# Performance work log

Hardware: AMD Instinct MI355X
Metric: run time of the kernel (lower is better)

## Reference

```python
import jax, jax.numpy as jnp
import numpy as np

# Sheet geometry: 256x256 neurons, 32 random synapses + 1 self synapse per neuron
R, C, S, STD, B = 256, 256, 32, 10.0, 64
N = R * C
NNZ = N * (S + 1)


def _build_indices(seed=0):
    """Replicates the torch constructor: per neuron (i,j), draw S gaussian
    2D offsets (std=STD), truncate to int, clamp to the sheet, linearize as
    i*C + j, and append the neuron's own index (self synapse).
    A[row=synapse, col=root] so out = A @ x^T scatters into synapse locations.
    """
    rng = np.random.default_rng(seed)
    ii, jj = np.meshgrid(np.arange(R), np.arange(C), indexing='ij')
    centers = np.stack([ii.ravel(), jj.ravel()], axis=1)           # [N, 2]
    syn = (rng.standard_normal((N, 2, S)) * STD
           + centers[:, :, None]).astype(np.int64)                 # trunc like .long()
    syn[:, 0] = np.clip(syn[:, 0], 0, R - 1)
    syn[:, 1] = np.clip(syn[:, 1], 0, C - 1)
    lin = syn[:, 0] * C + syn[:, 1]                                # [N, S]
    rows = np.concatenate([lin, np.arange(N)[:, None]], axis=1).ravel()  # [NNZ]
    cols = np.repeat(np.arange(N), S + 1)                          # [NNZ]
    return rows, cols


def setup_inputs() -> dict:
    key = jax.random.key(0)
    k1, k2 = jax.random.split(key)
    rows, cols = _build_indices()
    # He initialization: randn * sqrt(2 / synapses_per_neuron)
    values = jax.random.normal(k1, (NNZ,), dtype=jnp.float32) * np.float32(np.sqrt(2.0 / S))
    x = jax.random.normal(k2, (B, N), dtype=jnp.float32)  # batch_first
    return {"x": x, "values": values,
            "rows": jnp.asarray(rows, dtype=jnp.int64 if jax.config.jax_enable_x64 else jnp.int32),
            "cols": jnp.asarray(cols, dtype=jnp.int64 if jax.config.jax_enable_x64 else jnp.int32)}


def reference(x, values, rows, cols):
    # Sparse mm: out = A @ x^T with A[rows[e], cols[e]] += values[e]
    # (coalescing duplicates in torch_sparse sums values; segment_sum is equivalent)
    xt = x.T                                   # [N, B]
    gathered = xt[cols]                        # [NNZ, B] gather by root neuron
    out = jax.ops.segment_sum(values[:, None] * gathered, rows,
                              num_segments=N)  # [N, B] scatter to synapse rows
    return out.T                               # back to batch_first [B, N]
```

## Files before the change

### kernel.cpp

```cpp
#include <hip/hip_runtime.h>
#include <stdint.h>

#define N_NEUR  65536
#define NNZ_E   2162688
#define NBUK    4096
#define BSH     4
#define BROWS   16
#define EPB     4096
#define NBLK_E  (NNZ_E / EPB)
#define CHUNK   1536
#define EBUFSZ  (CHUNK + BROWS * 8)


__device__ inline unsigned short f2bf(float f) {
  const uint32_t u = __float_as_uint(f);
  return (unsigned short)((u + 0x7FFFu + ((u >> 16) & 1u)) >> 16);
}

__global__ __launch_bounds__(256) void k_front(const float* __restrict__ x,
                                               unsigned short* __restrict__ xtb,
                                               const int* __restrict__ rows,
                                               int* __restrict__ bcnt) {
  __shared__ float smem[64 * 65];
  const int t = threadIdx.x;
  if (blockIdx.x < 1024) {
    float (*tile)[65] = (float (*)[65])smem;
    const int n0 = blockIdx.x * 64;
    const int lane = t & 63;
    const int w = t >> 6;
    #pragma unroll
    for (int bb = w; bb < 64; bb += 4)
      tile[bb][lane] = x[(size_t)bb * N_NEUR + n0 + lane];
    __syncthreads();
    #pragma unroll
    for (int nn = w; nn < 64; nn += 4)
      xtb[(size_t)(n0 + nn) * 64 + lane] = f2bf(tile[lane][nn]);
  } else {
    int* lh = (int*)smem;
    #pragma unroll
    for (int q = 0; q < NBUK / 256; ++q) lh[q * 256 + t] = 0;
    __syncthreads();
    const int e0 = (blockIdx.x - 1024) * EPB;
    #pragma unroll
    for (int k = 0; k < EPB / 256; ++k)
      atomicAdd(&lh[rows[e0 + k * 256 + t] >> BSH], 1);
    __syncthreads();
    #pragma unroll
    for (int q = 0; q < NBUK / 256; ++q) {
      const int v = lh[q * 256 + t];
      if (v) atomicAdd(&bcnt[q * 256 + t], v);
    }
  }
}

__device__ inline int wave_incl_scan(int v, int lane) {
  #pragma unroll
  for (int off = 1; off < 64; off <<= 1) {
    int tv = __shfl_up(v, off, 64);
    if (lane >= off) v += tv;
  }
  return v;
}

__global__ __launch_bounds__(256) void k_bscan(const int* __restrict__ bcnt,
                                               int* __restrict__ boffs,
                                               int* __restrict__ gcur) {
  const int t = threadIdx.x, lane = t & 63, w = t >> 6;
  int c[16], s = 0;
  #pragma unroll
  for (int k = 0; k < 16; ++k) { c[k] = bcnt[t * 16 + k]; s += c[k]; }
  int incl = wave_incl_scan(s, lane);
  __shared__ int wsum[4];
  if (lane == 63) wsum[w] = incl;
  __syncthreads();
  int base = 0;
  for (int i = 0; i < w; ++i) base += wsum[i];
  int run = base + incl - s;
  #pragma unroll
  for (int k = 0; k < 16; ++k) {
    boffs[t * 16 + k] = run;
    gcur[t * 16 + k]  = run;
    run += c[k];
  }
}

__global__ __launch_bounds__(256) void k_bin(const int* __restrict__ rows,
                                             const float* __restrict__ vals,
                                             int* __restrict__ gcur,
                                             uint64_t* __restrict__ csr) {
  __shared__ int lc[NBUK];
  __shared__ int lofs[NBUK];
  __shared__ int wsum[4];
  __shared__ uint64_t ebuf[EPB];
  const int t = threadIdx.x, lane = t & 63, w = t >> 6;
  #pragma unroll
  for (int q = 0; q < NBUK / 256; ++q) lc[q * 256 + t] = 0;
  __syncthreads();
  const int e0 = blockIdx.x * EPB;
  int rcache[EPB / 256];
  #pragma unroll
  for (int k = 0; k < EPB / 256; ++k) {
    const int r = rows[e0 + k * 256 + t];
    rcache[k] = r;
    atomicAdd(&lc[r >> BSH], 1);
  }
  __syncthreads();
  {
    int c[16], s = 0;
    #pragma unroll
    for (int k = 0; k < 16; ++k) { c[k] = lc[t * 16 + k]; s += c[k]; }
    int incl = wave_incl_scan(s, lane);
    if (lane == 63) wsum[w] = incl;
    __syncthreads();
    int base = 0;
    for (int i = 0; i < w; ++i) base += wsum[i];
    int run = base + incl - s;
    #pragma unroll
    for (int k = 0; k < 16; ++k) { lofs[t * 16 + k] = run; run += c[k]; }
  }
  __syncthreads();
  #pragma unroll
  for (int q = 0; q < NBUK / 256; ++q) {
    const int bb = q * 256 + t;
    const int c = lc[bb];
    if (c) lc[bb] = atomicAdd(&gcur[bb], c) - lofs[bb];
  }
  __syncthreads();
  #pragma unroll
  for (int k = 0; k < EPB / 256; ++k) {
    const int e = e0 + k * 256 + t;
    const int r = rcache[k];
    const uint32_t c = (uint32_t)e / 33u;
    const uint64_t pk = ((uint64_t)__float_as_uint(vals[e]) << 32) |
                        ((uint32_t)r << 16) | c;
    const int pos = atomicAdd(&lofs[r >> BSH], 1);
    ebuf[pos] = pk;
  }
  __syncthreads();
  #pragma unroll
  for (int k = 0; k < EPB / 256; ++k) {
    const int idx = k * 256 + t;
    const uint64_t pk = ebuf[idx];
    const int bb = (int)((pk >> (16 + BSH)) & (NBUK - 1));
    csr[lc[bb] + idx] = pk;
  }
}

__global__ __launch_bounds__(256) void k_gather(const unsigned short* __restrict__ xtb,
                                                const int* __restrict__ boffs,
                                                const int* __restrict__ bcnt,
                                                const uint64_t* __restrict__ csr,
                                                float* __restrict__ out) {
  __shared__ uint64_t ebuf[EBUFSZ];
  __shared__ float tile[BROWS][66];
  __shared__ int lhist[BROWS], lofs[BROWS], lcur[BROWS], lpc[BROWS];
  const int t = threadIdx.x, lane = t & 63, w = t >> 6;
  const int h = lane >> 5, p = lane & 31;
  const int bid = blockIdx.x;
  const int g = (bid & 7) * (NBUK / 8) + (bid >> 3);
  const int r0 = g * BROWS;
  const int beg = boffs[g];
  const int cnt = bcnt[g];
  const uint32_t* __restrict__ xtu = (const uint32_t*)xtb;

  float accx[4] = {0.f, 0.f, 0.f, 0.f};
  float accy[4] = {0.f, 0.f, 0.f, 0.f};

  for (int c0 = 0; c0 < cnt; c0 += CHUNK) {
    const int len = (cnt - c0 < CHUNK) ? (cnt - c0) : CHUNK;
    if (t < BROWS) lhist[t] = 0;
    __syncthreads();
    uint64_t E[CHUNK / 256];
    #pragma unroll
    for (int u = 0; u < CHUNK / 256; ++u) {
      const int i = u * 256 + t;
      if (i < len) {
        const uint64_t e = csr[beg + c0 + i];
        E[u] = e;
        atomicAdd(&lhist[(int)((e >> 16) & (BROWS - 1))], 1);
      }
    }
    __syncthreads();
    if (t == 0) {
      int run = 0;
      #pragma unroll
      for (int r = 0; r < BROWS; ++r) {
        const int c = lhist[r];
        const int pc = (c + 7) & ~7;
        lofs[r] = run; lcur[r] = run; lpc[r] = pc;
        run += pc;
      }
    }
    __syncthreads();
    if (t < 128) {
      const int r = t >> 3, pi = t & 7;
      const int c = lhist[r];
      if (pi < lpc[r] - c) ebuf[lofs[r] + c + pi] = 0ULL;
    }
    #pragma unroll
    for (int u = 0; u < CHUNK / 256; ++u) {
      const int i = u * 256 + t;
      if (i < len) {
        const int rlo = (int)((E[u] >> 16) & (BROWS - 1));
        const int pos = atomicAdd(&lcur[rlo], 1);
        ebuf[pos] = E[u];
      }
    }
    __syncthreads();
    #pragma unroll
    for (int q = 0; q < 4; ++q) {
      const int rlo = w * 4 + q;
      const int s = __builtin_amdgcn_readfirstlane(lofs[rlo]);
      const int npair = __builtin_amdgcn_readfirstlane(lpc[rlo]) >> 1;
      float ax = 0.f, ay = 0.f, bx = 0.f, by = 0.f;
      int ti = 0;
      for (; ti + 8 <= npair; ti += 8) {
        uint64_t e[8]; uint32_t xv[8];
        #pragma unroll
        for (int u = 0; u < 8; ++u) e[u] = ebuf[s + 2 * (ti + u) + h];
        #pragma unroll
        for (int u = 0; u < 8; ++u)
          xv[u] = xtu[(int)(e[u] & 0xFFFF) * 32 + p];
        #pragma unroll
        for (int u = 0; u < 8; ++u) {
          const float v  = __uint_as_float((uint32_t)(e[u] >> 32));
          const float lo = __uint_as_float(xv[u] << 16);
          const float hi = __uint_as_float(xv[u] & 0xFFFF0000u);
          if (u & 1) { bx = fmaf(v, lo, bx); by = fmaf(v, hi, by); }
          else       { ax = fmaf(v, lo, ax); ay = fmaf(v, hi, ay); }
        }
      }
      if (ti < npair) {
        uint64_t e[4]; uint32_t xv[4];
        #pragma unroll
        for (int u = 0; u < 4; ++u) e[u] = ebuf[s + 2 * (ti + u) + h];
        #pragma unroll
        for (int u = 0; u < 4; ++u)
          xv[u] = xtu[(int)(e[u] & 0xFFFF) * 32 + p];
        #pragma unroll
        for (int u = 0; u < 4; ++u) {
          const float v  = __uint_as_float((uint32_t)(e[u] >> 32));
          const float lo = __uint_as_float(xv[u] << 16);
          const float hi = __uint_as_float(xv[u] & 0xFFFF0000u);
          if (u & 1) { bx = fmaf(v, lo, bx); by = fmaf(v, hi, by); }
          else       { ax = fmaf(v, lo, ax); ay = fmaf(v, hi, ay); }
        }
      }
      accx[q] += ax + bx;
      accy[q] += ay + by;
    }
    __syncthreads();
  }

  #pragma unroll
  for (int q = 0; q < 4; ++q) {
    float sx = accx[q] + __shfl_xor(accx[q], 32, 64);
    float sy = accy[q] + __shfl_xor(accy[q], 32, 64);
    if (h == 0) {
      tile[w * 4 + q][2 * p]     = sx;
      tile[w * 4 + q][2 * p + 1] = sy;
    }
  }
  __syncthreads();
  #pragma unroll
  for (int pp = 0; pp < (BROWS * 64) / 256; ++pp) {
    const int idx = pp * 256 + t;
    const int bb = idx >> 4;
    const int rl = idx & (BROWS - 1);
    out[(size_t)bb * N_NEUR + r0 + rl] = tile[rl][bb];
  }
}

extern "C" void kernel_launch(void* const* d_in, const int* in_sizes, int n_in,
                              void* d_out, int out_size, void* d_ws, size_t ws_size,
                              hipStream_t stream) {
  const float* x    = (const float*)d_in[0];
  const float* vals = (const float*)d_in[1];
  const int*   rows = (const int*)d_in[2];
  float* out = (float*)d_out;

  char* ws = (char*)d_ws;
  unsigned short* xtb = (unsigned short*)(ws + 0);
  int*      bcnt  = (int*)     (ws + 16777216);
  int*      boffs = (int*)     (ws + 16793600);
  int*      gcur  = (int*)     (ws + 16809984);
  uint64_t* csr   = (uint64_t*)(ws + 16826368);

  hipMemsetAsync(bcnt, 0, NBUK * sizeof(int), stream);
  k_front<<<1024 + NBLK_E, 256, 0, stream>>>(x, xtb, rows, bcnt);
  k_bscan<<<1, 256, 0, stream>>>(bcnt, boffs, gcur);
  k_bin<<<NBLK_E, 256, 0, stream>>>(rows, vals, gcur, csr);
  k_gather<<<NBUK, 256, 0, stream>>>(xtb, boffs, bcnt, csr, out);
}
```

Measured before the change: 88.30 us.

## Split row sort into separate kernel, fold bucket scan into binning, balance gather waves

The global bucket scan is folded into every k_bin block, which removes the single-block k_bscan launch. A new k_bin2 kernel sorts each bucket's edges by row into a padded csr2 array. k_gather then streams presorted entries with 128-bit loads and splits the work evenly across its four waves, flushing per-row partial sums through shared-memory atomics. Buckets are also mapped to blocks in an interleaved front/back order. The aims are to cut the sort and sync overhead inside the gather and to balance load across waves, at the cost of an extra kernel pass over the edges. There is also a new risk: k_bin2 clamps buckets to CAP (4096) entries, so larger buckets would silently drop edges.

```diff
diff --git a/kernel.cpp b/kernel.cpp
--- a/kernel.cpp
+++ b/kernel.cpp
@@ -8,13 +8,18 @@
 #define BROWS   16
 #define EPB     4096
 #define NBLK_E  (NNZ_E / EPB)
-#define CHUNK   1536
-#define EBUFSZ  (CHUNK + BROWS * 8)
+#define CAP     4096
 
 
 __device__ inline unsigned short f2bf(float f) {
   const uint32_t u = __float_as_uint(f);
   return (unsigned short)((u + 0x7FFFu + ((u >> 16) & 1u)) >> 16);
+}
+
+__device__ inline int bucket_of_block(int bid) {
+  const int l = bid >> 3;
+  const int lf = (l & 1) ? (511 - (l >> 1)) : (l >> 1);
+  return (bid & 7) * 512 + lf;
 }
 
 __global__ __launch_bounds__(256) void k_front(const float* __restrict__ x,
@@ -62,37 +67,42 @@
   return v;
 }
 
-__global__ __launch_bounds__(256) void k_bscan(const int* __restrict__ bcnt,
-                                               int* __restrict__ boffs,
-                                               int* __restrict__ gcur) {
-  const int t = threadIdx.x, lane = t & 63, w = t >> 6;
-  int c[16], s = 0;
-  #pragma unroll
-  for (int k = 0; k < 16; ++k) { c[k] = bcnt[t * 16 + k]; s += c[k]; }
-  int incl = wave_incl_scan(s, lane);
-  __shared__ int wsum[4];
-  if (lane == 63) wsum[w] = incl;
-  __syncthreads();
-  int base = 0;
-  for (int i = 0; i < w; ++i) base += wsum[i];
-  int run = base + incl - s;
-  #pragma unroll
-  for (int k = 0; k < 16; ++k) {
-    boffs[t * 16 + k] = run;
-    gcur[t * 16 + k]  = run;
-    run += c[k];
-  }
-}
-
 __global__ __launch_bounds__(256) void k_bin(const int* __restrict__ rows,
                                              const float* __restrict__ vals,
+                                             const int* __restrict__ bcnt,
+                                             int* __restrict__ boffs,
                                              int* __restrict__ gcur,
-                                             uint64_t* __restrict__ csr) {
+                                             uint64_t* __restrict__ csr1) {
   __shared__ int lc[NBUK];
   __shared__ int lofs[NBUK];
   __shared__ int wsum[4];
   __shared__ uint64_t ebuf[EPB];
   const int t = threadIdx.x, lane = t & 63, w = t >> 6;
+
+  int* sc = (int*)ebuf;
+  #pragma unroll
+  for (int q = 0; q < NBUK / 256; ++q) sc[q * 256 + t] = bcnt[q * 256 + t];
+  __syncthreads();
+  int gb[16];
+  {
+    int gs = 0;
+    #pragma unroll
+    for (int k = 0; k < 16; ++k) { gb[k] = sc[t * 16 + k]; gs += gb[k]; }
+    int incl = wave_incl_scan(gs, lane);
+    if (lane == 63) wsum[w] = incl;
+    __syncthreads();
+    int base = 0;
+    for (int i = 0; i < w; ++i) base += wsum[i];
+    int run = base + incl - gs;
+    #pragma unroll
+    for (int k = 0; k < 16; ++k) { const int c = gb[k]; gb[k] = run; run += c; }
+  }
+  if (blockIdx.x == 0) {
+    #pragma unroll
+    for (int k = 0; k < 16; ++k) boffs[t * 16 + k] = gb[k];
+  }
+  __syncthreads();
+
   #pragma unroll
   for (int q = 0; q < NBUK / 256; ++q) lc[q * 256 + t] = 0;
   __syncthreads();
@@ -120,10 +130,10 @@
   }
   __syncthreads();
   #pragma unroll
-  for (int q = 0; q < NBUK / 256; ++q) {
-    const int bb = q * 256 + t;
+  for (int k = 0; k < 16; ++k) {
+    const int bb = t * 16 + k;
     const int c = lc[bb];
-    if (c) lc[bb] = atomicAdd(&gcur[bb], c) - lofs[bb];
+    if (c) lc[bb] = gb[k] + atomicAdd(&gcur[bb], c) - lofs[bb];
   }
   __syncthreads();
   #pragma unroll
@@ -142,125 +152,156 @@
     const int idx = k * 256 + t;
     const uint64_t pk = ebuf[idx];
     const int bb = (int)((pk >> (16 + BSH)) & (NBUK - 1));
-    csr[lc[bb] + idx] = pk;
-  }
+    csr1[lc[bb] + idx] = pk;
+  }
+}
+
+__global__ __launch_bounds__(256) void k_bin2(const int* __restrict__ bcnt,
+                                              const int* __restrict__ boffs,
+                                              const uint64_t* __restrict__ csr1,
+                                              uint64_t* __restrict__ csr2,
+                                              int* __restrict__ rowbase,
+                                              int* __restrict__ pcnt) {
+  __shared__ uint64_t ebuf[CAP + BROWS * 8];
+  __shared__ int lh[BROWS], lofs[BROWS], lcur[BROWS], lpc[BROWS];
+  __shared__ int ptot_s;
+  const int t = threadIdx.x;
+  const int g = bucket_of_block(blockIdx.x);
+  const int beg = boffs[g];
+  int cnt = bcnt[g];
+  if (cnt > CAP) cnt = CAP;
+  if (t < BROWS) lh[t] = 0;
+  __syncthreads();
+  uint64_t E[CAP / 256];
+  #pragma unroll
+  for (int u = 0; u < CAP / 256; ++u) {
+    const int i = u * 256 + t;
+    if (i < cnt) {
+      const uint64_t e = csr1[beg + i];
+      E[u] = e;
+      atomicAdd(&lh[(int)((e >> 16) & (BROWS - 1))], 1);
+    }
+  }
+  __syncthreads();
+  if (t == 0) {
+    int run = 0;
+    #pragma unroll
+    for (int r = 0; r < BROWS; ++r) {
+      const int c = lh[r];
+      const int pc = (c + 7) & ~7;
+      lofs[r] = run; lcur[r] = run; lpc[r] = pc;
+      run += pc;
+    }
+    ptot_s = run;
+  }
+  __syncthreads();
+  if (t < 128) {
+    const int r = t >> 3, pi = t & 7;
+    const int c = lh[r];
+    if (pi < lpc[r] - c) ebuf[lofs[r] + c + pi] = 0ULL;
+  }
+  #pragma unroll
+  for (int u = 0; u < CAP / 256; ++u) {
+    const int i = u * 256 + t;
+    if (i < cnt) {
+      const int rlo = (int)((E[u] >> 16) & (BROWS - 1));
+      const int pos = atomicAdd(&lcur[rlo], 1);
+      ebuf[pos] = E[u];
+    }
+  }
+  __syncthreads();
+  const int base2 = (beg + g * 128 + 1) & ~1;
+  const int ptot = ptot_s;
+  for (int i = t; i < ptot; i += 256)
+    csr2[base2 + i] = ebuf[i];
+  if (t == 0) { rowbase[g] = base2; pcnt[g] = ptot; }
 }
 
 __global__ __launch_bounds__(256) void k_gather(const unsigned short* __restrict__ xtb,
-                                                const int* __restrict__ boffs,
-                                                const int* __restrict__ bcnt,
-                                                const uint64_t* __restrict__ csr,
+                                                const int* __restrict__ rowbase,
+                                                const int* __restrict__ pcnt,
+                                                const uint64_t* __restrict__ csr2,
                                                 float* __restrict__ out) {
-  __shared__ uint64_t ebuf[EBUFSZ];
   __shared__ float tile[BROWS][66];
-  __shared__ int lhist[BROWS], lofs[BROWS], lcur[BROWS], lpc[BROWS];
   const int t = threadIdx.x, lane = t & 63, w = t >> 6;
   const int h = lane >> 5, p = lane & 31;
-  const int bid = blockIdx.x;
-  const int g = (bid & 7) * (NBUK / 8) + (bid >> 3);
+  const int g = bucket_of_block(blockIdx.x);
   const int r0 = g * BROWS;
-  const int beg = boffs[g];
-  const int cnt = bcnt[g];
+  const int base2 = __builtin_amdgcn_readfirstlane(rowbase[g]);
+  const int nw = __builtin_amdgcn_readfirstlane(pcnt[g]) >> 3;
+  const ulonglong2* __restrict__ ep2 = (const ulonglong2*)csr2 + (base2 >> 1);
   const uint32_t* __restrict__ xtu = (const uint32_t*)xtb;
 
-  float accx[4] = {0.f, 0.f, 0.f, 0.f};
-  float accy[4] = {0.f, 0.f, 0.f, 0.f};
-
-  for (int c0 = 0; c0 < cnt; c0 += CHUNK) {
-    const int len = (cnt - c0 < CHUNK) ? (cnt - c0) : CHUNK;
-    if (t < BROWS) lhist[t] = 0;
-    __syncthreads();
-    uint64_t E[CHUNK / 256];
-    #pragma unroll
-    for (int u = 0; u < CHUNK / 256; ++u) {
-      const int i = u * 256 + t;
-      if (i < len) {
-        const uint64_t e = csr[beg + c0 + i];
-        E[u] = e;
-        atomicAdd(&lhist[(int)((e >> 16) & (BROWS - 1))], 1);
-      }
-    }
-    __syncthreads();
-    if (t == 0) {
-      int run = 0;
-      #pragma unroll
-      for (int r = 0; r < BROWS; ++r) {
-        const int c = lhist[r];
-        const int pc = (c + 7) & ~7;
-        lofs[r] = run; lcur[r] = run; lpc[r] = pc;
-        run += pc;
-      }
-    }
-    __syncthreads();
-    if (t < 128) {
-      const int r = t >> 3, pi = t & 7;
-      const int c = lhist[r];
-      if (pi < lpc[r] - c) ebuf[lofs[r] + c + pi] = 0ULL;
-    }
-    #pragma unroll
-    for (int u = 0; u < CHUNK / 256; ++u) {
-      const int i = u * 256 + t;
-      if (i < len) {
-        const int rlo = (int)((E[u] >> 16) & (BROWS - 1));
-        const int pos = atomicAdd(&lcur[rlo], 1);
-        ebuf[pos] = E[u];
-      }
-    }
-    __syncthreads();
-    #pragma unroll
-    for (int q = 0; q < 4; ++q) {
-      const int rlo = w * 4 + q;
-      const int s = __builtin_amdgcn_readfirstlane(lofs[rlo]);
-      const int npair = __builtin_amdgcn_readfirstlane(lpc[rlo]) >> 1;
-      float ax = 0.f, ay = 0.f, bx = 0.f, by = 0.f;
-      int ti = 0;
-      for (; ti + 8 <= npair; ti += 8) {
-        uint64_t e[8]; uint32_t xv[8];
-        #pragma unroll
-        for (int u = 0; u < 8; ++u) e[u] = ebuf[s + 2 * (ti + u) + h];
-        #pragma unroll
-        for (int u = 0; u < 8; ++u)
-          xv[u] = xtu[(int)(e[u] & 0xFFFF) * 32 + p];
-        #pragma unroll
-        for (int u = 0; u < 8; ++u) {
-          const float v  = __uint_as_float((uint32_t)(e[u] >> 32));
-          const float lo = __uint_as_float(xv[u] << 16);
-          const float hi = __uint_as_float(xv[u] & 0xFFFF0000u);
-          if (u & 1) { bx = fmaf(v, lo, bx); by = fmaf(v, hi, by); }
-          else       { ax = fmaf(v, lo, ax); ay = fmaf(v, hi, ay); }
-        }
-      }
-      if (ti < npair) {
-        uint64_t e[4]; uint32_t xv[4];
-        #pragma unroll
-        for (int u = 0; u < 4; ++u) e[u] = ebuf[s + 2 * (ti + u) + h];
-        #pragma unroll
-        for (int u = 0; u < 4; ++u)
-          xv[u] = xtu[(int)(e[u] & 0xFFFF) * 32 + p];
-        #pragma unroll
-        for (int u = 0; u < 4; ++u) {
-          const float v  = __uint_as_float((uint32_t)(e[u] >> 32));
-          const float lo = __uint_as_float(xv[u] << 16);
-          const float hi = __uint_as_float(xv[u] & 0xFFFF0000u);
-          if (u & 1) { bx = fmaf(v, lo, bx); by = fmaf(v, hi, by); }
-          else       { ax = fmaf(v, lo, ax); ay = fmaf(v, hi, ay); }
-        }
-      }
-      accx[q] += ax + bx;
-      accy[q] += ay + by;
-    }
-    __syncthreads();
-  }
-
-  #pragma unroll
-  for (int q = 0; q < 4; ++q) {
-    float sx = accx[q] + __shfl_xor(accx[q], 32, 64);
-    float sy = accy[q] + __shfl_xor(accy[q], 32, 64);
-    if (h == 0) {
-      tile[w * 4 + q][2 * p]     = sx;
-      tile[w * 4 + q][2 * p + 1] = sy;
-    }
-  }
+  for (int i = t; i < BROWS * 66; i += 256) ((float*)tile)[i] = 0.f;
+  __syncthreads();
+
+  const int wi0 = (nw * w) >> 2;
+  const int wi1 = (nw * (w + 1)) >> 2;
+  float ax = 0.f, ay = 0.f, bx = 0.f, by = 0.f;
+  int cur = -1;
+
+#define FLUSH()                                                          \
+  {                                                                      \
+    float sx = ax + bx; sx += __shfl_xor(sx, 32, 64);                    \
+    float sy = ay + by; sy += __shfl_xor(sy, 32, 64);                    \
+    if (h == 0) {                                                        \
+      atomicAdd(&tile[cur][2 * p], sx);                                  \
+      atomicAdd(&tile[cur][2 * p + 1], sy);                              \
+    }                                                                    \
+    ax = ay = bx = by = 0.f;                                             \
+  }
+
+  int wi = wi0;
+  for (; wi + 2 <= wi1; wi += 2) {
+    ulonglong2 qq[8]; uint64_t e[8]; uint32_t xv[8];
+    #pragma unroll
+    for (int u = 0; u < 8; ++u) qq[u] = ep2[wi * 4 + u];
+    #pragma unroll
+    for (int u = 0; u < 8; ++u) e[u] = h ? qq[u].y : qq[u].x;
+    #pragma unroll
+    for (int u = 0; u < 8; ++u) xv[u] = xtu[(int)(e[u] & 0xFFFF) * 32 + p];
+    const int rowA = (int)((qq[0].x >> 16) & (BROWS - 1));
+    const int rowB = (int)((qq[4].x >> 16) & (BROWS - 1));
+    if (rowA != cur) { if (cur >= 0) FLUSH(); cur = rowA; }
+    #pragma unroll
+    for (int u = 0; u < 4; ++u) {
+      const float v  = __uint_as_float((uint32_t)(e[u] >> 32));
+      const float lo = __uint_as_float(xv[u] << 16);
+      const float hi = __uint_as_float(xv[u] & 0xFFFF0000u);
+      if (u & 1) { bx = fmaf(v, lo, bx); by = fmaf(v, hi, by); }
+      else       { ax = fmaf(v, lo, ax); ay = fmaf(v, hi, ay); }
+    }
+    if (rowB != cur) { FLUSH(); cur = rowB; }
+    #pragma unroll
+    for (int u = 4; u < 8; ++u) {
+      const float v  = __uint_as_float((uint32_t)(e[u] >> 32));
+      const float lo = __uint_as_float(xv[u] << 16);
+      const float hi = __uint_as_float(xv[u] & 0xFFFF0000u);
+      if (u & 1) { bx = fmaf(v, lo, bx); by = fmaf(v, hi, by); }
+      else       { ax = fmaf(v, lo, ax); ay = fmaf(v, hi, ay); }
+    }
+  }
+  if (wi < wi1) {
+    ulonglong2 qq[4]; uint64_t e[4]; uint32_t xv[4];
+    #pragma unroll
+    for (int u = 0; u < 4; ++u) qq[u] = ep2[wi * 4 + u];
+    #pragma unroll
+    for (int u = 0; u < 4; ++u) e[u] = h ? qq[u].y : qq[u].x;
+    #pragma unroll
+    for (int u = 0; u < 4; ++u) xv[u] = xtu[(int)(e[u] & 0xFFFF) * 32 + p];
+    const int rowA = (int)((qq[0].x >> 16) & (BROWS - 1));
+    if (rowA != cur) { if (cur >= 0) FLUSH(); cur = rowA; }
+    #pragma unroll
+    for (int u = 0; u < 4; ++u) {
+      const float v  = __uint_as_float((uint32_t)(e[u] >> 32));
+      const float lo = __uint_as_float(xv[u] << 16);
+      const float hi = __uint_as_float(xv[u] & 0xFFFF0000u);
+      if (u & 1) { bx = fmaf(v, lo, bx); by = fmaf(v, hi, by); }
+      else       { ax = fmaf(v, lo, ax); ay = fmaf(v, hi, ay); }
+    }
+  }
+  if (cur >= 0) FLUSH();
+#undef FLUSH
   __syncthreads();
   #pragma unroll
   for (int pp = 0; pp < (BROWS * 64) / 256; ++pp) {
@@ -280,15 +321,18 @@
   float* out = (float*)d_out;
 
   char* ws = (char*)d_ws;
-  unsigned short* xtb = (unsigned short*)(ws + 0);
-  int*      bcnt  = (int*)     (ws + 16777216);
-  int*      boffs = (int*)     (ws + 16793600);
-  int*      gcur  = (int*)     (ws + 16809984);
-  uint64_t* csr   = (uint64_t*)(ws + 16826368);
-
-  hipMemsetAsync(bcnt, 0, NBUK * sizeof(int), stream);
+  unsigned short* xtb     = (unsigned short*)(ws + 0);
+  int*            pcnt    = (int*)     (ws + 8388608);
+  int*            rowbase = (int*)     (ws + 8404992);
+  int*            bcnt    = (int*)     (ws + 16777216);
+  int*            boffs   = (int*)     (ws + 16793600);
+  int*            gcur    = (int*)     (ws + 16809984);
+  uint64_t*       csr1    = (uint64_t*)(ws + 16826368);
+  uint64_t*       csr2    = (uint64_t*)(ws + 34127872);
+
+  hipMemsetAsync(bcnt, 0, 3 * NBUK * sizeof(int), stream);
   k_front<<<1024 + NBLK_E, 256, 0, stream>>>(x, xtb, rows, bcnt);
-  k_bscan<<<1, 256, 0, stream>>>(bcnt, boffs, gcur);
-  k_bin<<<NBLK_E, 256, 0, stream>>>(rows, vals, gcur, csr);
-  k_gather<<<NBUK, 256, 0, stream>>>(xtb, boffs, bcnt, csr, out);
-}
+  k_bin<<<NBLK_E, 256, 0, stream>>>(rows, vals, bcnt, boffs, gcur, csr1);
+  k_bin2<<<NBUK, 256, 0, stream>>>(bcnt, boffs, csr1, csr2, rowbase, pcnt);
+  k_gather<<<NBUK, 256, 0, stream>>>(xtb, rowbase, pcnt, csr2, out);
+}
```

After: 337.9 us. 283% more time.

## Fold bucket prefix scan into binning kernel and reorder gather block mapping

Applied to the files above, without the earlier changes.

Removes the single-block k_bscan launch. Each k_bin block now redundantly scans the 4096 global bucket counts in shared memory, and block 0 writes boffs. gcur becomes a zeroed relative cursor that the memset clears, so the memset now covers three arrays. The gather block-to-bucket mapping is also changed to interleave buckets from the front and back of each segment, which should balance load or improve locality. The trade-off is a redundant 16KB read and scan in every binning block in exchange for one fewer launch and dependency.

```diff
diff --git a/kernel.cpp b/kernel.cpp
--- a/kernel.cpp
+++ b/kernel.cpp
@@ -15,6 +15,12 @@
 __device__ inline unsigned short f2bf(float f) {
   const uint32_t u = __float_as_uint(f);
   return (unsigned short)((u + 0x7FFFu + ((u >> 16) & 1u)) >> 16);
+}
+
+__device__ inline int bucket_of_block(int bid) {
+  const int l = bid >> 3;
+  const int lf = (l & 1) ? (511 - (l >> 1)) : (l >> 1);
+  return (bid & 7) * 512 + lf;
 }
 
 __global__ __launch_bounds__(256) void k_front(const float* __restrict__ x,
@@ -62,30 +68,10 @@
   return v;
 }
 
-__global__ __launch_bounds__(256) void k_bscan(const int* __restrict__ bcnt,
-                                               int* __restrict__ boffs,
-                                               int* __restrict__ gcur) {
-  const int t = threadIdx.x, lane = t & 63, w = t >> 6;
-  int c[16], s = 0;
-  #pragma unroll
-  for (int k = 0; k < 16; ++k) { c[k] = bcnt[t * 16 + k]; s += c[k]; }
-  int incl = wave_incl_scan(s, lane);
-  __shared__ int wsum[4];
-  if (lane == 63) wsum[w] = incl;
-  __syncthreads();
-  int base = 0;
-  for (int i = 0; i < w; ++i) base += wsum[i];
-  int run = base + incl - s;
-  #pragma unroll
-  for (int k = 0; k < 16; ++k) {
-    boffs[t * 16 + k] = run;
-    gcur[t * 16 + k]  = run;
-    run += c[k];
-  }
-}
-
 __global__ __launch_bounds__(256) void k_bin(const int* __restrict__ rows,
                                              const float* __restrict__ vals,
+                                             const int* __restrict__ bcnt,
+                                             int* __restrict__ boffs,
                                              int* __restrict__ gcur,
                                              uint64_t* __restrict__ csr) {
   __shared__ int lc[NBUK];
@@ -93,6 +79,31 @@
   __shared__ int wsum[4];
   __shared__ uint64_t ebuf[EPB];
   const int t = threadIdx.x, lane = t & 63, w = t >> 6;
+
+  int* sc = (int*)ebuf;
+  #pragma unroll
+  for (int q = 0; q < NBUK / 256; ++q) sc[q * 256 + t] = bcnt[q * 256 + t];
+  __syncthreads();
+  int gb[16];
+  {
+    int gs = 0;
+    #pragma unroll
+    for (int k = 0; k < 16; ++k) { gb[k] = sc[t * 16 + k]; gs += gb[k]; }
+    int incl = wave_incl_scan(gs, lane);
+    if (lane == 63) wsum[w] = incl;
+    __syncthreads();
+    int base = 0;
+    for (int i = 0; i < w; ++i) base += wsum[i];
+    int run = base + incl - gs;
+    #pragma unroll
+    for (int k = 0; k < 16; ++k) { const int c = gb[k]; gb[k] = run; run += c; }
+  }
+  if (blockIdx.x == 0) {
+    #pragma unroll
+    for (int k = 0; k < 16; ++k) boffs[t * 16 + k] = gb[k];
+  }
+  __syncthreads();
+
   #pragma unroll
   for (int q = 0; q < NBUK / 256; ++q) lc[q * 256 + t] = 0;
   __syncthreads();
@@ -120,10 +131,10 @@
   }
   __syncthreads();
   #pragma unroll
-  for (int q = 0; q < NBUK / 256; ++q) {
-    const int bb = q * 256 + t;
+  for (int k = 0; k < 16; ++k) {
+    const int bb = t * 16 + k;
     const int c = lc[bb];
-    if (c) lc[bb] = atomicAdd(&gcur[bb], c) - lofs[bb];
+    if (c) lc[bb] = gb[k] + atomicAdd(&gcur[bb], c) - lofs[bb];
   }
   __syncthreads();
   #pragma unroll
@@ -156,8 +167,7 @@
   __shared__ int lhist[BROWS], lofs[BROWS], lcur[BROWS], lpc[BROWS];
   const int t = threadIdx.x, lane = t & 63, w = t >> 6;
   const int h = lane >> 5, p = lane & 31;
-  const int bid = blockIdx.x;
-  const int g = (bid & 7) * (NBUK / 8) + (bid >> 3);
+  const int g = bucket_of_block(blockIdx.x);
   const int r0 = g * BROWS;
   const int beg = boffs[g];
   const int cnt = bcnt[g];
@@ -286,9 +296,8 @@
   int*      gcur  = (int*)     (ws + 16809984);
   uint64_t* csr   = (uint64_t*)(ws + 16826368);
 
-  hipMemsetAsync(bcnt, 0, NBUK * sizeof(int), stream);
+  hipMemsetAsync(bcnt, 0, 3 * NBUK * sizeof(int), stream);
   k_front<<<1024 + NBLK_E, 256, 0, stream>>>(x, xtb, rows, bcnt);
-  k_bscan<<<1, 256, 0, stream>>>(bcnt, boffs, gcur);
-  k_bin<<<NBLK_E, 256, 0, stream>>>(rows, vals, gcur, csr);
+  k_bin<<<NBLK_E, 256, 0, stream>>>(rows, vals, bcnt, boffs, gcur, csr);
   k_gather<<<NBUK, 256, 0, stream>>>(xtb, boffs, bcnt, csr, out);
 }
```

Result: slower. 96.99 us (+9.8%).
